# Kernel optimization log

Measured on AMD Instinct MI355X. Metric: run time of the kernel, lower is better.

## Reference

```python
import jax, jax.numpy as jnp
import numpy as np

H = 64      # h_dim
E = 64      # embedding_dim
L = 100     # latent_dim
T = 30      # seq_len
DT = 0.03

def _leaky(x):
    return jnp.where(x >= 0, x, 0.01 * x)  # nn.LeakyReLU default slope

def _mlp(h, Ws, bs, Wf, bf):
    # 3 stacked [H,H] LeakyReLU layers + final [L,H] layer, LeakyReLU after EVERY layer (as in source)
    for i in range(Ws.shape[0]):
        h = _leaky(h @ Ws[i].T + bs[i])
    return _leaky(h @ Wf.T + bf)

def _lstm_step(h, c, gates):
    # torch LSTM gate order: i, f, g, o
    i, f, g, o = jnp.split(gates, 4, axis=-1)
    c = jax.nn.sigmoid(f) * c + jax.nn.sigmoid(i) * jnp.tanh(g)
    h = jax.nn.sigmoid(o) * jnp.tanh(c)
    return h, c

def _forward(expert_traj, init_state, eps,
             W_se, b_se,
             W_ih_e, W_hh_e, b_ih_e, b_hh_e,
             mean_Ws, mean_bs, mean_Wf, mean_bf,
             lv_Ws, lv_bs, lv_Wf, lv_bf,
             W_init, b_init,
             W_ih_d, W_hh_d, b_ih_d, b_hh_d,
             W_c, b_c):
    B = expert_traj.shape[0]
    # --- encode: relative positions ---
    rel_xy = jnp.concatenate([expert_traj[:, :1, :2],
                              expert_traj[:, 1:, :2] - expert_traj[:, :-1, :2]], axis=1)
    inp = jnp.concatenate([rel_xy, expert_traj[:, :, 2:]], axis=-1)  # [B,T,4]
    emb = inp @ W_se.T + b_se                                        # [B,T,E]
    x_seq = jnp.swapaxes(emb, 0, 1)                                  # [T,B,E] seq-major
    # precompute input projection for all timesteps in one GEMM
    xp = x_seq @ W_ih_e.T + (b_ih_e + b_hh_e)                        # [T,B,4H]
    h0 = jnp.zeros((B, H), dtype=expert_traj.dtype)
    c0 = jnp.zeros((B, H), dtype=expert_traj.dtype)
    def enc_step(carry, xp_t):
        h, c = carry
        h, c = _lstm_step(h, c, xp_t + h @ W_hh_e.T)
        return (h, c), None
    (hT, _), _ = jax.lax.scan(enc_step, (h0, c0), xp)
    mu = _mlp(hT, mean_Ws, mean_bs, mean_Wf, mean_bf)                # [B,L]
    log_var = _mlp(hT, lv_Ws, lv_bs, lv_Wf, lv_bf)                   # [B,L]
    # --- reparameterize + tanh ---
    z = jnp.tanh(eps * jnp.exp(0.5 * log_var) + mu)
    # --- decode ---
    dh = z @ W_init.T + b_init                                       # [B,H], h0 = c0 = dh
    bias_d = b_ih_d + b_hh_d
    def dec_step(carry, _):
        h, c, prev = carry
        xe = prev @ W_se.T + b_se                                    # spatial embedding of state
        h, c = _lstm_step(h, c, xe @ W_ih_d.T + h @ W_hh_d.T + bias_d)
        ctrl = h @ W_c.T + b_c                                       # [B,2]
        pedal = ctrl[:, 0]
        steer = jnp.clip(ctrl[:, 1], -0.5, 0.5)
        x_t, y_t, psi, v = prev[:, 0], prev[:, 1], prev[:, 2], prev[:, 3]
        v1 = jnp.clip(v + pedal * DT, 0.0, 30.0)
        psi_dot = jnp.clip(v * jnp.tan(steer) / 2.5, -3.14 / 2, 3.14 / 2)
        cur = jnp.stack([x_t + v * jnp.cos(psi) * DT,
                         y_t + v * jnp.sin(psi) * DT,
                         psi + psi_dot * DT,
                         v1], axis=1)
        return (h, c, cur), cur
    _, traj = jax.lax.scan(dec_step, (dh, dh, init_state), None, length=T)
    recons = jnp.swapaxes(traj, 0, 1)                                # [B,T,4]
    return recons, expert_traj, mu, log_var

def setup_inputs() -> dict:
    key = jax.random.key(0)
    ks = jax.random.split(key, 32)
    B = 16384
    s = 0.05
    def p(k, shape):
        return jax.random.normal(k, shape, dtype=jnp.float32) * s
    return {
        "expert_traj": jax.random.normal(ks[0], (B, T, 4), dtype=jnp.float32),
        "init_state": jax.random.normal(ks[1], (B, 4), dtype=jnp.float32),
        "eps": jax.random.normal(ks[2], (B, L), dtype=jnp.float32),
        "W_se": p(ks[3], (E, 4)), "b_se": p(ks[4], (E,)),
        "W_ih_e": p(ks[5], (4 * H, E)), "W_hh_e": p(ks[6], (4 * H, H)),
        "b_ih_e": p(ks[7], (4 * H,)), "b_hh_e": p(ks[8], (4 * H,)),
        "mean_Ws": p(ks[9], (3, H, H)), "mean_bs": p(ks[10], (3, H)),
        "mean_Wf": p(ks[11], (L, H)), "mean_bf": p(ks[12], (L,)),
        "lv_Ws": p(ks[13], (3, H, H)), "lv_bs": p(ks[14], (3, H)),
        "lv_Wf": p(ks[15], (L, H)), "lv_bf": p(ks[16], (L,)),
        "W_init": p(ks[17], (H, L)), "b_init": p(ks[18], (H,)),
        "W_ih_d": p(ks[19], (4 * H, E)), "W_hh_d": p(ks[20], (4 * H, H)),
        "b_ih_d": p(ks[21], (4 * H,)), "b_hh_d": p(ks[22], (4 * H,)),
        "W_c": p(ks[23], (2, H)), "b_c": p(ks[24], (2,)),
    }

def reference(expert_traj, init_state, eps,
              W_se, b_se,
              W_ih_e, W_hh_e, b_ih_e, b_hh_e,
              mean_Ws, mean_bs, mean_Wf, mean_bf,
              lv_Ws, lv_bs, lv_Wf, lv_bf,
              W_init, b_init,
              W_ih_d, W_hh_d, b_ih_d, b_hh_d,
              W_c, b_c):
    return _forward(expert_traj, init_state, eps,
                    W_se, b_se,
                    W_ih_e, W_hh_e, b_ih_e, b_hh_e,
                    mean_Ws, mean_bs, mean_Wf, mean_bf,
                    lv_Ws, lv_bs, lv_Wf, lv_bf,
                    W_init, b_init,
                    W_ih_d, W_hh_d, b_ih_d, b_hh_d,
                    W_c, b_c)
```

## Files before the change

kernel.cpp:

```cpp
#include <hip/hip_runtime.h>

typedef unsigned short u16;
typedef unsigned int u32;
typedef __attribute__((ext_vector_type(8))) short bf16x8;
typedef __attribute__((ext_vector_type(4))) float f32x4;

#define B_TOT 16384
#define RR 16
#define BLK 128
#define NBLK (B_TOT / RR)
#define TT 30
#define LL 100
#define DTC 0.03f
#define L2E 1.44269504088896f

#define HST 104
#define HBUF (RR * HST)

#define OFF_H   0
#define OFF_XS  6656
#define OFF_INP 10752
#define OFF_ZB  14592
#define SMEM_SZ 18944

#define WS_WHHE  0
#define WS_WHHD  18432
#define WS_MWS   36864
#define WS_LWS   49152
#define WS_MWF   61440
#define WS_LWF   67840
#define WS_WINIT 74240
#define WS_TOTAL 82432

__device__ __forceinline__ float bf2f(u16 u) {
    union { u32 i; float f; } v; v.i = ((u32)u) << 16; return v.f;
}
__device__ __forceinline__ u16 f2bf(float f) {
    union { float f; u32 i; } v; v.f = f;
    return (u16)((v.i + 0x7FFFu + ((v.i >> 16) & 1u)) >> 16);
}
__device__ __forceinline__ u16 f2bf_t(float f) {
    union { float f; u32 i; } v; v.f = f;
    return (u16)(v.i >> 16);
}
__device__ __forceinline__ float rcpf(float x) { return __builtin_amdgcn_rcpf(x); }
__device__ __forceinline__ float ex2(float x) { return __builtin_amdgcn_exp2f(x); }
__device__ __forceinline__ float tanh_(float x) {
    x = fminf(fmaxf(x, -15.f), 15.f);
    float e = __expf(2.f * x);
    return (e - 1.f) * rcpf(e + 1.f);
}
__device__ __forceinline__ float leaky(float x) { return x >= 0.f ? x : 0.01f * x; }
__device__ __forceinline__ f32x4 mfma16(bf16x8 a, bf16x8 b, f32x4 c) {
    return __builtin_amdgcn_mfma_f32_16x16x32_bf16(a, b, c, 0, 0, 0);
}

__global__ void setup_kernel(
    const float* __restrict__ W_se, const float* __restrict__ b_se,
    const float* __restrict__ W_ih_e, const float* __restrict__ W_hh_e,
    const float* __restrict__ b_ih_e, const float* __restrict__ b_hh_e,
    const float* __restrict__ W_ih_d, const float* __restrict__ W_hh_d,
    const float* __restrict__ b_ih_d, const float* __restrict__ b_hh_d,
    const float* __restrict__ mean_Ws, const float* __restrict__ lv_Ws,
    const float* __restrict__ mean_Wf, const float* __restrict__ lv_Wf,
    const float* __restrict__ W_init, u16* __restrict__ ws)
{
    const int gid = blockIdx.x * 256 + threadIdx.x;
    const int nth = gridDim.x * 256;
    for (int i = gid; i < 512; i += nth) {
        int which = i >> 8, row = i & 255, g = row >> 6;
        float s = (g == 2) ? 2.f * L2E : L2E;
        const float* wih = (which ? W_ih_d : W_ih_e) + row * 64;
        float f0=0,f1=0,f2=0,f3=0,fb=0;
        for (int e = 0; e < 64; ++e) {
            float w = wih[e];
            f0 = fmaf(w, W_se[e*4+0], f0);
            f1 = fmaf(w, W_se[e*4+1], f1);
            f2 = fmaf(w, W_se[e*4+2], f2);
            f3 = fmaf(w, W_se[e*4+3], f3);
            fb = fmaf(w, b_se[e], fb);
        }
        fb += (which ? b_ih_d : b_ih_e)[row] + (which ? b_hh_d : b_hh_e)[row];
        u16* dst = ws + (which ? WS_WHHD : WS_WHHE) + row * 72 + 64;
        dst[0]=f2bf(f0*s); dst[1]=f2bf(f1*s); dst[2]=f2bf(f2*s); dst[3]=f2bf(f3*s);
        dst[4]=f2bf(fb*s); dst[5]=0; dst[6]=0; dst[7]=0;
    }
    for (int i = gid; i < 2*16384; i += nth) {
        int which = i >= 16384;
        int j = which ? i - 16384 : i;
        int row = j >> 6, k = j & 63, g = row >> 6;
        float s = (g == 2) ? 2.f * L2E : L2E;
        const float* whh = which ? W_hh_d : W_hh_e;
        ws[(which ? WS_WHHD : WS_WHHE) + row*72 + k] = f2bf(whh[j] * s);
    }
    for (int i = gid; i < 12288; i += nth) {
        ws[WS_MWS + i] = f2bf(mean_Ws[i]);
        ws[WS_LWS + i] = f2bf(lv_Ws[i]);
    }
    for (int i = gid; i < 6400; i += nth) {
        ws[WS_MWF + i] = f2bf(mean_Wf[i]);
        ws[WS_LWF + i] = f2bf(lv_Wf[i]);
    }
    for (int i = gid; i < 8192; i += nth) {
        int r = i >> 7, k = i & 127;
        ws[WS_WINIT + i] = (k < LL) ? f2bf(W_init[r*LL + k]) : (u16)0;
    }
}

__global__ __launch_bounds__(BLK, 2) void vae_lstm_kernel(
    const float* __restrict__ expert, const float* __restrict__ init_state,
    const float* __restrict__ eps, const u16* __restrict__ ws,
    const float* __restrict__ mean_bs, const float* __restrict__ mean_bf,
    const float* __restrict__ lv_bs, const float* __restrict__ lv_bf,
    const float* __restrict__ b_init, const float* __restrict__ W_c,
    const float* __restrict__ b_c,
    float* __restrict__ out_recons, float* __restrict__ out_expert,
    float* __restrict__ out_mu, float* __restrict__ out_lv)
{
    const int tid = threadIdx.x;
    const int wv = tid >> 6;
    const int l = tid & 63;
    const int lcol = l & 15;
    const int quad = l >> 4;
    const int ubase = wv * 32;
    const int b0 = blockIdx.x * RR;

    __shared__ __align__(16) char smem[SMEM_SZ];
    u16* Hb  = (u16*)(smem + OFF_H);
    u16* XS  = (u16*)(smem + OFF_XS);
    u16* XA  = XS;
    u16* XB  = XS + RR*64;
    u16* inp = (u16*)(smem + OFF_INP);
    u16* zB  = (u16*)(smem + OFF_ZB);
    float* sc = (float*)XS;

    {
        u32* hz = (u32*)Hb;
        for (int idx = tid; idx < 2*RR*52; idx += BLK) hz[idx] = 0;
        u32* zz = (u32*)zB;
        for (int idx = tid; idx < RR*68; idx += BLK) zz[idx] = 0;
        __syncthreads();
        if (tid < 32) Hb[(tid >> 4)*HBUF + (tid & 15)*HST + 68] = 0x3F80;
        const int base = b0 * (TT*4);
        for (int idx = tid; idx < RR*TT*4; idx += BLK) {
            int row = idx / 120, q = idx % 120;
            int t = q >> 2, k = q & 3;
            float v = expert[base + idx];
            out_expert[base + idx] = v;
            float r = v;
            if (k < 2 && t > 0) r = v - expert[base + idx - 4];
            u16 hv = f2bf(r);
            inp[row*120 + q] = hv;
            if (t == 0) Hb[row*HST + 64 + k] = hv;
        }
        __syncthreads();
    }

    float cst[2][4] = {};
    float hval[2][4];
    bf16x8 bw[4][2][3];

    auto build_bw = [&](const u16* wsW) {
#pragma unroll
        for (int g = 0; g < 4; ++g)
#pragma unroll
            for (int ul = 0; ul < 2; ++ul) {
                const u16* wr = wsW + (g*64 + ubase + ul*16 + lcol) * 72;
                bw[g][ul][0] = *(const bf16x8*)(wr + quad*8);
                bw[g][ul][1] = *(const bf16x8*)(wr + 32 + quad*8);
                bw[g][ul][2] = *(const bf16x8*)(wr + 64);
            }
#pragma unroll
        for (int g = 0; g < 4; ++g)
#pragma unroll
            for (int ul = 0; ul < 2; ++ul)
#pragma unroll
                for (int kk = 0; kk < 3; ++kk)
                    asm volatile("" : "+v"(bw[g][ul][kk]));
    };

    auto lstm_step = [&](const u16* Hc, u16* Hn) {
        const u16* hrow = Hc + lcol*HST;
        bf16x8 a0 = *(const bf16x8*)(hrow + quad*8);
        bf16x8 a1 = *(const bf16x8*)(hrow + 32 + quad*8);
        bf16x8 a2 = *(const bf16x8*)(hrow + 64 + quad*8);
        f32x4 acc[4][2];
#pragma unroll
        for (int g = 0; g < 4; ++g)
#pragma unroll
            for (int ul = 0; ul < 2; ++ul) {
                f32x4 z = {0.f, 0.f, 0.f, 0.f};
                z = mfma16(a0, bw[g][ul][0], z);
                z = mfma16(a1, bw[g][ul][1], z);
                acc[g][ul] = mfma16(a2, bw[g][ul][2], z);
            }
#pragma unroll
        for (int ul = 0; ul < 2; ++ul)
#pragma unroll
            for (int r = 0; r < 4; ++r) {
                float Ei = ex2(-acc[0][ul][r]);
                float Ef = ex2(-acc[1][ul][r]);
                float Eg = ex2(-acc[2][ul][r]);
                float Eo = ex2(-acc[3][ul][r]);
                float P = (1.f + Ei) * (1.f + Eg);
                float Q = 1.f + Ef;
                float num = fmaf(cst[ul][r], P, (1.f - Eg) * Q);
                float cc = num * rcpf(P * Q);
                cst[ul][r] = cc;
                float Ec = ex2(-2.f * L2E * cc);
                float h = (1.f - Ec) * rcpf((1.f + Eo) * (1.f + Ec));
                hval[ul][r] = h;
                Hn[(quad*4 + r)*HST + ubase + ul*16 + lcol] = f2bf_t(h);
            }
    };

    build_bw(ws + WS_WHHE);
    for (int stp = 0; stp < TT; ++stp) {
        const u16* Hc = Hb + (stp & 1) * HBUF;
        u16* Hn = Hb + ((stp + 1) & 1) * HBUF;
        lstm_step(Hc, Hn);
        if (wv == 0 && stp < TT - 1) {
            int row = l >> 2, k = l & 3;
            Hn[row*HST + 64 + k] = inp[row*120 + (stp + 1)*4 + k];
        }
        __syncthreads();
    }
    u16* H0 = Hb;
    u16* H1 = Hb + HBUF;

    auto mlp_hidden = [&](const u16* inB, int ist, u16* outB, int ost,
                          const u16* wsW, const float* bg) {
        bf16x8 a0 = *(const bf16x8*)(inB + lcol*ist + quad*8);
        bf16x8 a1 = *(const bf16x8*)(inB + lcol*ist + 32 + quad*8);
#pragma unroll
        for (int ul = 0; ul < 2; ++ul) {
            int n = ubase + ul*16 + lcol;
            const u16* wr = wsW + n*64;
            bf16x8 bb0 = *(const bf16x8*)(wr + quad*8);
            bf16x8 bb1 = *(const bf16x8*)(wr + 32 + quad*8);
            float bv = bg[n];
            f32x4 acc = {bv, bv, bv, bv};
            acc = mfma16(a0, bb0, acc);
            acc = mfma16(a1, bb1, acc);
#pragma unroll
            for (int r = 0; r < 4; ++r)
                outB[(quad*4 + r)*ost + n] = f2bf_t(leaky(acc[r]));
        }
        __syncthreads();
    };

    mlp_hidden(H0, HST, XA, 64, ws + WS_MWS,        mean_bs);
    mlp_hidden(XA, 64,  XB, 64, ws + WS_MWS + 4096, mean_bs + 64);
    mlp_hidden(XB, 64,  XA, 64, ws + WS_MWS + 8192, mean_bs + 128);

    float muv[4][4];

    {
        bf16x8 fa = *(const bf16x8*)(XA + lcol*64 + quad*8);
        bf16x8 fb = *(const bf16x8*)(XA + lcol*64 + 32 + quad*8);
#pragma unroll
        for (int ti = 0; ti < 4; ++ti) {
            int nt = wv + ti*2;
            if (nt > 6) continue;
            int n = nt*16 + lcol;
            bool ok = (n < LL);
            bf16x8 bb0, bb1;
            if (ok) {
                const u16* wr = ws + WS_MWF + n*64;
                bb0 = *(const bf16x8*)(wr + quad*8);
                bb1 = *(const bf16x8*)(wr + 32 + quad*8);
            } else {
#pragma unroll
                for (int j = 0; j < 8; ++j) { bb0[j] = 0; bb1[j] = 0; }
            }
            float bv = ok ? mean_bf[n] : 0.f;
            f32x4 acc = {bv, bv, bv, bv};
            acc = mfma16(fa, bb0, acc);
            acc = mfma16(fb, bb1, acc);
#pragma unroll
            for (int r = 0; r < 4; ++r) {
                float vv = leaky(acc[r]);
                muv[ti][r] = vv;
                if (ok) out_mu[(size_t)(b0 + quad*4 + r) * LL + n] = vv;
            }
        }
    }

    mlp_hidden(H0, HST, H1, HST, ws + WS_LWS,        lv_bs);
    mlp_hidden(H1, HST, H0, HST, ws + WS_LWS + 4096, lv_bs + 64);
    mlp_hidden(H0, HST, H1, HST, ws + WS_LWS + 8192, lv_bs + 128);

    {
        bf16x8 fa = *(const bf16x8*)(H1 + lcol*HST + quad*8);
        bf16x8 fb = *(const bf16x8*)(H1 + lcol*HST + 32 + quad*8);
#pragma unroll
        for (int ti = 0; ti < 4; ++ti) {
            int nt = wv + ti*2;
            if (nt > 6) continue;
            int n = nt*16 + lcol;
            bool ok = (n < LL);
            bf16x8 bb0, bb1;
            if (ok) {
                const u16* wr = ws + WS_LWF + n*64;
                bb0 = *(const bf16x8*)(wr + quad*8);
                bb1 = *(const bf16x8*)(wr + 32 + quad*8);
            } else {
#pragma unroll
                for (int j = 0; j < 8; ++j) { bb0[j] = 0; bb1[j] = 0; }
            }
            float bv = ok ? lv_bf[n] : 0.f;
            f32x4 acc = {bv, bv, bv, bv};
            acc = mfma16(fa, bb0, acc);
            acc = mfma16(fb, bb1, acc);
#pragma unroll
            for (int r = 0; r < 4; ++r) {
                if (ok) {
                    float lv = leaky(acc[r]);
                    size_t gi = (size_t)(b0 + quad*4 + r) * LL + n;
                    out_lv[gi] = lv;
                    float zv = tanh_(fmaf(eps[gi], __expf(0.5f * lv), muv[ti][r]));
                    zB[(quad*4 + r)*136 + n] = f2bf_t(zv);
                }
            }
        }
        __syncthreads();
    }

    {
        bf16x8 az[4];
#pragma unroll
        for (int kt = 0; kt < 4; ++kt)
            az[kt] = *(const bf16x8*)(zB + lcol*136 + kt*32 + quad*8);
#pragma unroll
        for (int ul = 0; ul < 2; ++ul) {
            int n = ubase + ul*16 + lcol;
            float bv = b_init[n];
            f32x4 acc = {bv, bv, bv, bv};
#pragma unroll
            for (int kt = 0; kt < 4; ++kt) {
                bf16x8 bi = *(const bf16x8*)(ws + WS_WINIT + n*128 + kt*32 + quad*8);
                acc = mfma16(az[kt], bi, acc);
            }
#pragma unroll
            for (int r = 0; r < 4; ++r) {
                cst[ul][r] = acc[r];
                H0[(quad*4 + r)*HST + n] = f2bf_t(acc[r]);
            }
        }
    }

    if (wv == 0) {
        int row = l >> 2, k = l & 3;
        H0[row*HST + 64 + k] = f2bf(init_state[(size_t)(b0 + row)*4 + k]);
    }
    float px = 0.f, py = 0.f, ppsi = 0.f, pv = 0.f;
    if (tid < 16) {
        const float* is = init_state + (size_t)(b0 + tid)*4;
        px = is[0]; py = is[1]; ppsi = is[2]; pv = is[3];
    }
    float wc0[2], wc1[2];
#pragma unroll
    for (int ul = 0; ul < 2; ++ul) {
        wc0[ul] = W_c[ubase + ul*16 + lcol];
        wc1[ul] = W_c[64 + ubase + ul*16 + lcol];
    }
    const float bc0 = b_c[0], bc1 = b_c[1];
    build_bw(ws + WS_WHHD);
    __syncthreads();

    for (int stp = 0; stp < TT; ++stp) {
        const u16* Hc = Hb + (stp & 1) * HBUF;
        u16* Hn = Hb + ((stp + 1) & 1) * HBUF;
        lstm_step(Hc, Hn);
        float pa[4], pb[4];
#pragma unroll
        for (int r = 0; r < 4; ++r) {
            pa[r] = fmaf(hval[0][r], wc0[0], hval[1][r] * wc0[1]);
            pb[r] = fmaf(hval[0][r], wc1[0], hval[1][r] * wc1[1]);
        }
#pragma unroll
        for (int d = 1; d < 16; d <<= 1) {
#pragma unroll
            for (int r = 0; r < 4; ++r) {
                pa[r] += __shfl_xor(pa[r], d);
                pb[r] += __shfl_xor(pb[r], d);
            }
        }
        if (lcol == 0) {
#pragma unroll
            for (int r = 0; r < 4; ++r) {
                sc[wv*32 + quad*4 + r]      = pa[r];
                sc[wv*32 + 16 + quad*4 + r] = pb[r];
            }
        }
        __syncthreads();
        if (tid < 16) {
            int row = tid;
            float pedal = sc[row] + sc[32 + row] + bc0;
            float steer = fminf(fmaxf(sc[16 + row] + sc[48 + row] + bc1, -0.5f), 0.5f);
            float v1 = fminf(fmaxf(pv + pedal * DTC, 0.f), 30.f);
            float sn, cs;
            __sincosf(ppsi, &sn, &cs);
            float psid = fminf(fmaxf(pv * __tanf(steer) * 0.4f, -1.57f), 1.57f);
            float nx = fmaf(pv * cs, DTC, px);
            float ny = fmaf(pv * sn, DTC, py);
            float npsi = fmaf(psid, DTC, ppsi);
            px = nx; py = ny; ppsi = npsi; pv = v1;
            float4 o; o.x = nx; o.y = ny; o.z = npsi; o.w = v1;
            *(float4*)(out_recons + ((size_t)(b0 + row) * TT + stp) * 4) = o;
            u32 lo = (u32)f2bf(nx) | ((u32)f2bf(ny) << 16);
            u32 hi = (u32)f2bf(npsi) | ((u32)f2bf(v1) << 16);
            uint2 pk; pk.x = lo; pk.y = hi;
            *(uint2*)(Hn + row*HST + 64) = pk;
        }
        __syncthreads();
    }
}

extern "C" void kernel_launch(void* const* d_in, const int* in_sizes, int n_in,
                              void* d_out, int out_size, void* d_ws, size_t ws_size,
                              hipStream_t stream) {
    (void)in_sizes; (void)n_in; (void)ws_size; (void)out_size;
    const float* expert    = (const float*)d_in[0];
    const float* init_st   = (const float*)d_in[1];
    const float* eps       = (const float*)d_in[2];
    const float* W_se      = (const float*)d_in[3];
    const float* b_se      = (const float*)d_in[4];
    const float* W_ih_e    = (const float*)d_in[5];
    const float* W_hh_e    = (const float*)d_in[6];
    const float* b_ih_e    = (const float*)d_in[7];
    const float* b_hh_e    = (const float*)d_in[8];
    const float* mean_Ws   = (const float*)d_in[9];
    const float* mean_bs   = (const float*)d_in[10];
    const float* mean_Wf   = (const float*)d_in[11];
    const float* mean_bf   = (const float*)d_in[12];
    const float* lv_Ws     = (const float*)d_in[13];
    const float* lv_bs     = (const float*)d_in[14];
    const float* lv_Wf     = (const float*)d_in[15];
    const float* lv_bf     = (const float*)d_in[16];
    const float* W_init    = (const float*)d_in[17];
    const float* b_init    = (const float*)d_in[18];
    const float* W_ih_d    = (const float*)d_in[19];
    const float* W_hh_d    = (const float*)d_in[20];
    const float* b_ih_d    = (const float*)d_in[21];
    const float* b_hh_d    = (const float*)d_in[22];
    const float* W_c       = (const float*)d_in[23];
    const float* b_c       = (const float*)d_in[24];

    float* out = (float*)d_out;
    const size_t n_traj = (size_t)B_TOT * TT * 4;
    const size_t n_lat  = (size_t)B_TOT * LL;
    float* out_recons = out;
    float* out_expert = out + n_traj;
    float* out_mu     = out + 2 * n_traj;
    float* out_lv     = out + 2 * n_traj + n_lat;

    u16* ws = (u16*)d_ws;

    setup_kernel<<<64, 256, 0, stream>>>(
        W_se, b_se, W_ih_e, W_hh_e, b_ih_e, b_hh_e,
        W_ih_d, W_hh_d, b_ih_d, b_hh_d,
        mean_Ws, lv_Ws, mean_Wf, lv_Wf, W_init, ws);

    vae_lstm_kernel<<<NBLK, BLK, 0, stream>>>(
        expert, init_st, eps, ws,
        mean_bs, mean_bf, lv_bs, lv_bf, b_init, W_c, b_c,
        out_recons, out_expert, out_mu, out_lv);
}
```

Before: 228.7 us.

## Split each block's hidden units across four waves instead of two

The block grows from 128 to 256 threads while keeping the same 16 batch rows, so each wave now owns 16 hidden units instead of 32. The LSTM recurrence, MLP layers, init projection and output-head reduction are all re-indexed for one unit tile per wave, and the cross-wave partial-sum reduction now adds four slots. The aim is to halve each wave's serial MFMA and transcendental chain per timestep and put more waves in flight to hide latency in this latency-bound recurrent loop. The cost is more threads joining every block barrier, and a launch bound that asks for four blocks per CU, which tightens the register budget.

```diff
diff --git a/kernel.cpp b/kernel.cpp
--- a/kernel.cpp
+++ b/kernel.cpp
@@ -7,7 +7,7 @@
 
 #define B_TOT 16384
 #define RR 16
-#define BLK 128
+#define BLK 256
 #define NBLK (B_TOT / RR)
 #define TT 30
 #define LL 100
@@ -107,7 +107,7 @@
     }
 }
 
-__global__ __launch_bounds__(BLK, 2) void vae_lstm_kernel(
+__global__ __launch_bounds__(BLK, 4) void vae_lstm_kernel(
     const float* __restrict__ expert, const float* __restrict__ init_state,
     const float* __restrict__ eps, const u16* __restrict__ ws,
     const float* __restrict__ mean_bs, const float* __restrict__ mean_bf,
@@ -122,7 +122,7 @@
     const int l = tid & 63;
     const int lcol = l & 15;
     const int quad = l >> 4;
-    const int ubase = wv * 32;
+    const int ubase = wv * 16;
     const int b0 = blockIdx.x * RR;
 
     __shared__ __align__(16) char smem[SMEM_SZ];
@@ -156,27 +156,23 @@
         __syncthreads();
     }
 
-    float cst[2][4] = {};
-    float hval[2][4];
-    bf16x8 bw[4][2][3];
+    float cst[4] = {};
+    float hval[4];
+    bf16x8 bw[4][3];
 
     auto build_bw = [&](const u16* wsW) {
 #pragma unroll
+        for (int g = 0; g < 4; ++g) {
+            const u16* wr = wsW + (g*64 + ubase + lcol) * 72;
+            bw[g][0] = *(const bf16x8*)(wr + quad*8);
+            bw[g][1] = *(const bf16x8*)(wr + 32 + quad*8);
+            bw[g][2] = *(const bf16x8*)(wr + 64);
+        }
+#pragma unroll
         for (int g = 0; g < 4; ++g)
 #pragma unroll
-            for (int ul = 0; ul < 2; ++ul) {
-                const u16* wr = wsW + (g*64 + ubase + ul*16 + lcol) * 72;
-                bw[g][ul][0] = *(const bf16x8*)(wr + quad*8);
-                bw[g][ul][1] = *(const bf16x8*)(wr + 32 + quad*8);
-                bw[g][ul][2] = *(const bf16x8*)(wr + 64);
-            }
-#pragma unroll
-        for (int g = 0; g < 4; ++g)
-#pragma unroll
-            for (int ul = 0; ul < 2; ++ul)
-#pragma unroll
-                for (int kk = 0; kk < 3; ++kk)
-                    asm volatile("" : "+v"(bw[g][ul][kk]));
+            for (int kk = 0; kk < 3; ++kk)
+                asm volatile("" : "+v"(bw[g][kk]));
     };
 
     auto lstm_step = [&](const u16* Hc, u16* Hn) {
@@ -184,34 +180,30 @@
         bf16x8 a0 = *(const bf16x8*)(hrow + quad*8);
         bf16x8 a1 = *(const bf16x8*)(hrow + 32 + quad*8);
         bf16x8 a2 = *(const bf16x8*)(hrow + 64 + quad*8);
-        f32x4 acc[4][2];
-#pragma unroll
-        for (int g = 0; g < 4; ++g)
-#pragma unroll
-            for (int ul = 0; ul < 2; ++ul) {
-                f32x4 z = {0.f, 0.f, 0.f, 0.f};
-                z = mfma16(a0, bw[g][ul][0], z);
-                z = mfma16(a1, bw[g][ul][1], z);
-                acc[g][ul] = mfma16(a2, bw[g][ul][2], z);
-            }
-#pragma unroll
-        for (int ul = 0; ul < 2; ++ul)
-#pragma unroll
-            for (int r = 0; r < 4; ++r) {
-                float Ei = ex2(-acc[0][ul][r]);
-                float Ef = ex2(-acc[1][ul][r]);
-                float Eg = ex2(-acc[2][ul][r]);
-                float Eo = ex2(-acc[3][ul][r]);
-                float P = (1.f + Ei) * (1.f + Eg);
-                float Q = 1.f + Ef;
-                float num = fmaf(cst[ul][r], P, (1.f - Eg) * Q);
-                float cc = num * rcpf(P * Q);
-                cst[ul][r] = cc;
-                float Ec = ex2(-2.f * L2E * cc);
-                float h = (1.f - Ec) * rcpf((1.f + Eo) * (1.f + Ec));
-                hval[ul][r] = h;
-                Hn[(quad*4 + r)*HST + ubase + ul*16 + lcol] = f2bf_t(h);
-            }
+        f32x4 acc[4];
+#pragma unroll
+        for (int g = 0; g < 4; ++g) {
+            f32x4 z = {0.f, 0.f, 0.f, 0.f};
+            z = mfma16(a0, bw[g][0], z);
+            z = mfma16(a1, bw[g][1], z);
+            acc[g] = mfma16(a2, bw[g][2], z);
+        }
+#pragma unroll
+        for (int r = 0; r < 4; ++r) {
+            float Ei = ex2(-acc[0][r]);
+            float Ef = ex2(-acc[1][r]);
+            float Eg = ex2(-acc[2][r]);
+            float Eo = ex2(-acc[3][r]);
+            float P = (1.f + Ei) * (1.f + Eg);
+            float Q = 1.f + Ef;
+            float num = fmaf(cst[r], P, (1.f - Eg) * Q);
+            float cc = num * rcpf(P * Q);
+            cst[r] = cc;
+            float Ec = ex2(-2.f * L2E * cc);
+            float h = (1.f - Ec) * rcpf((1.f + Eo) * (1.f + Ec));
+            hval[r] = h;
+            Hn[(quad*4 + r)*HST + ubase + lcol] = f2bf_t(h);
+        }
     };
 
     build_bw(ws + WS_WHHE);
@@ -219,8 +211,8 @@
         const u16* Hc = Hb + (stp & 1) * HBUF;
         u16* Hn = Hb + ((stp + 1) & 1) * HBUF;
         lstm_step(Hc, Hn);
-        if (wv == 0 && stp < TT - 1) {
-            int row = l >> 2, k = l & 3;
+        if (tid < 64 && stp < TT - 1) {
+            int row = tid >> 2, k = tid & 3;
             Hn[row*HST + 64 + k] = inp[row*120 + (stp + 1)*4 + k];
         }
         __syncthreads();
@@ -232,20 +224,17 @@
                           const u16* wsW, const float* bg) {
         bf16x8 a0 = *(const bf16x8*)(inB + lcol*ist + quad*8);
         bf16x8 a1 = *(const bf16x8*)(inB + lcol*ist + 32 + quad*8);
-#pragma unroll
-        for (int ul = 0; ul < 2; ++ul) {
-            int n = ubase + ul*16 + lcol;
-            const u16* wr = wsW + n*64;
-            bf16x8 bb0 = *(const bf16x8*)(wr + quad*8);
-            bf16x8 bb1 = *(const bf16x8*)(wr + 32 + quad*8);
-            float bv = bg[n];
-            f32x4 acc = {bv, bv, bv, bv};
-            acc = mfma16(a0, bb0, acc);
-            acc = mfma16(a1, bb1, acc);
-#pragma unroll
-            for (int r = 0; r < 4; ++r)
-                outB[(quad*4 + r)*ost + n] = f2bf_t(leaky(acc[r]));
-        }
+        int n = ubase + lcol;
+        const u16* wr = wsW + n*64;
+        bf16x8 bb0 = *(const bf16x8*)(wr + quad*8);
+        bf16x8 bb1 = *(const bf16x8*)(wr + 32 + quad*8);
+        float bv = bg[n];
+        f32x4 acc = {bv, bv, bv, bv};
+        acc = mfma16(a0, bb0, acc);
+        acc = mfma16(a1, bb1, acc);
+#pragma unroll
+        for (int r = 0; r < 4; ++r)
+            outB[(quad*4 + r)*ost + n] = f2bf_t(leaky(acc[r]));
         __syncthreads();
     };
 
@@ -253,14 +242,14 @@
     mlp_hidden(XA, 64,  XB, 64, ws + WS_MWS + 4096, mean_bs + 64);
     mlp_hidden(XB, 64,  XA, 64, ws + WS_MWS + 8192, mean_bs + 128);
 
-    float muv[4][4];
+    float muv[2][4];
 
     {
         bf16x8 fa = *(const bf16x8*)(XA + lcol*64 + quad*8);
         bf16x8 fb = *(const bf16x8*)(XA + lcol*64 + 32 + quad*8);
 #pragma unroll
-        for (int ti = 0; ti < 4; ++ti) {
-            int nt = wv + ti*2;
+        for (int ti = 0; ti < 2; ++ti) {
+            int nt = wv + ti*4;
             if (nt > 6) continue;
             int n = nt*16 + lcol;
             bool ok = (n < LL);
@@ -294,8 +283,8 @@
         bf16x8 fa = *(const bf16x8*)(H1 + lcol*HST + quad*8);
         bf16x8 fb = *(const bf16x8*)(H1 + lcol*HST + 32 + quad*8);
 #pragma unroll
-        for (int ti = 0; ti < 4; ++ti) {
-            int nt = wv + ti*2;
+        for (int ti = 0; ti < 2; ++ti) {
+            int nt = wv + ti*4;
             if (nt > 6) continue;
             int n = nt*16 + lcol;
             bool ok = (n < LL);
@@ -331,26 +320,23 @@
 #pragma unroll
         for (int kt = 0; kt < 4; ++kt)
             az[kt] = *(const bf16x8*)(zB + lcol*136 + kt*32 + quad*8);
-#pragma unroll
-        for (int ul = 0; ul < 2; ++ul) {
-            int n = ubase + ul*16 + lcol;
-            float bv = b_init[n];
-            f32x4 acc = {bv, bv, bv, bv};
-#pragma unroll
-            for (int kt = 0; kt < 4; ++kt) {
-                bf16x8 bi = *(const bf16x8*)(ws + WS_WINIT + n*128 + kt*32 + quad*8);
-                acc = mfma16(az[kt], bi, acc);
-            }
-#pragma unroll
-            for (int r = 0; r < 4; ++r) {
-                cst[ul][r] = acc[r];
-                H0[(quad*4 + r)*HST + n] = f2bf_t(acc[r]);
-            }
-        }
-    }
-
-    if (wv == 0) {
-        int row = l >> 2, k = l & 3;
+        int n = ubase + lcol;
+        float bv = b_init[n];
+        f32x4 acc = {bv, bv, bv, bv};
+#pragma unroll
+        for (int kt = 0; kt < 4; ++kt) {
+            bf16x8 bi = *(const bf16x8*)(ws + WS_WINIT + n*128 + kt*32 + quad*8);
+            acc = mfma16(az[kt], bi, acc);
+        }
+#pragma unroll
+        for (int r = 0; r < 4; ++r) {
+            cst[r] = acc[r];
+            H0[(quad*4 + r)*HST + n] = f2bf_t(acc[r]);
+        }
+    }
+
+    if (tid < 64) {
+        int row = tid >> 2, k = tid & 3;
         H0[row*HST + 64 + k] = f2bf(init_state[(size_t)(b0 + row)*4 + k]);
     }
     float px = 0.f, py = 0.f, ppsi = 0.f, pv = 0.f;
@@ -358,12 +344,8 @@
         const float* is = init_state + (size_t)(b0 + tid)*4;
         px = is[0]; py = is[1]; ppsi = is[2]; pv = is[3];
     }
-    float wc0[2], wc1[2];
-#pragma unroll
-    for (int ul = 0; ul < 2; ++ul) {
-        wc0[ul] = W_c[ubase + ul*16 + lcol];
-        wc1[ul] = W_c[64 + ubase + ul*16 + lcol];
-    }
+    const float wc0 = W_c[ubase + lcol];
+    const float wc1 = W_c[64 + ubase + lcol];
     const float bc0 = b_c[0], bc1 = b_c[1];
     build_bw(ws + WS_WHHD);
     __syncthreads();
@@ -375,8 +357,8 @@
         float pa[4], pb[4];
 #pragma unroll
         for (int r = 0; r < 4; ++r) {
-            pa[r] = fmaf(hval[0][r], wc0[0], hval[1][r] * wc0[1]);
-            pb[r] = fmaf(hval[0][r], wc1[0], hval[1][r] * wc1[1]);
+            pa[r] = hval[r] * wc0;
+            pb[r] = hval[r] * wc1;
         }
 #pragma unroll
         for (int d = 1; d < 16; d <<= 1) {
@@ -396,8 +378,9 @@
         __syncthreads();
         if (tid < 16) {
             int row = tid;
-            float pedal = sc[row] + sc[32 + row] + bc0;
-            float steer = fminf(fmaxf(sc[16 + row] + sc[48 + row] + bc1, -0.5f), 0.5f);
+            float pedal = sc[row] + sc[32 + row] + sc[64 + row] + sc[96 + row] + bc0;
+            float s1 = sc[16 + row] + sc[48 + row] + sc[80 + row] + sc[112 + row] + bc1;
+            float steer = fminf(fmaxf(s1, -0.5f), 0.5f);
             float v1 = fminf(fmaxf(pv + pedal * DTC, 0.f), 30.f);
             float sn, cs;
             __sincosf(ppsi, &sn, &cs);
```

Measured after the change: 233.6 us. 2.1% more time.
